# Kernel optimization log

Hardware: AMD Instinct MI355X
Metric: run time of the kernel (lower is better)

The kernel has to match this reference:

```python
import jax, jax.numpy as jnp
import numpy as np

B, H, D = 1, 24, 128
TXT, REDUX, IMG, REF, ROUTER, NC = 512, 64, 2048, 512, 32, 2
S = TXT + REDUX + IMG + REF + ROUTER
REF_SHIFT = 1.5  # model_config['ref_shift'] (nonzero to exercise the mask path)


def setup_inputs() -> dict:
    rng = jax.random.key(0)
    k1, k2, k3, k4, k5 = jax.random.split(rng, 5)
    tri = TXT + REDUX + IMG
    return {
        "query": jax.random.normal(k1, (B, H, S, D), jnp.float32),
        "key": jax.random.normal(k2, (B, H, S, D), jnp.float32),
        "value": jax.random.normal(k3, (B, H, S, D), jnp.float32),
        "ref_mask": jax.random.uniform(k4, (B, REF, tri), jnp.float32),
        "routing_map": jax.random.uniform(k5, (B, NC, IMG), jnp.float32),
        "txt_seq_len": TXT,
        "redux_seq_len": REDUX,
        "img_seq_len": IMG,
        "ref_seq_len": REF,
        "router_seq_len": ROUTER,
        "num_conds": NC,
    }


def _sdpa(q, k, v, mask=None):
    # torch F.scaled_dot_product_attention semantics (additive mask)
    scale = 1.0 / jnp.sqrt(jnp.asarray(q.shape[-1], q.dtype))
    logits = jnp.einsum('...qd,...kd->...qk', q, k) * scale
    if mask is not None:
        logits = logits + mask  # mask broadcasts over heads
    return jnp.einsum('...qk,...kd->...qd', jax.nn.softmax(logits, axis=-1), v)


def reference(query, key, value, ref_mask, routing_map,
              txt_seq_len, redux_seq_len, img_seq_len, ref_seq_len,
              router_seq_len, num_conds):
    b = query.shape[0]
    te = txt_seq_len                 # text end
    tre = te + redux_seq_len         # text+redux end
    tri = tre + img_seq_len          # text+redux+image end
    trir = tri + ref_seq_len         # +ref end

    # ---- additive attention mask (only the used [:tri, :trir] slice; broadcast over heads)
    mask = jnp.zeros((b, 1, tri, trir), query.dtype)
    mask = mask.at[:, :, :tri, tri:trir].add(REF_SHIFT)
    # ref_mask: [B, ref, tri] -> transpose -> [B, 1, tri, ref], (m-1)*100
    rm = (jnp.swapaxes(ref_mask, -1, -2)[:, None] - 1.0) * 100.0
    mask = mask.at[:, :, :tri, tri:trir].add(rm)
    # routing map for redux keys: [B, nc, img] -> repeat per-cond -> [B, redux, img] -> [B,1,img,redux]
    rep = redux_seq_len // num_conds
    redux_rt = (jnp.repeat(routing_map, rep, axis=1) - 1.0) * 100.0
    mask = mask.at[:, :, tre:tri, te:tre].add(jnp.swapaxes(redux_rt, 1, 2)[:, None])
    # routing map for ref keys: [B, nc, img] -> [B, ref, img] -> [B,1,img,ref]
    rep = ref_seq_len // num_conds
    ref_rt = (jnp.repeat(routing_map, rep, axis=1) - 1.0) * 100.0
    mask = mask.at[:, :, tre:tri, tri:trir].add(jnp.swapaxes(ref_rt, 1, 2)[:, None])

    # ---- segment 1: text+redux+image queries attend to text+redux+image+ref keys
    out1 = _sdpa(query[:, :, :tri], key[:, :, :trir], value[:, :, :trir], mask)

    # ---- segment 2: per-condition ref self-attention (block-diagonal over num_conds)
    h = query.shape[1]
    rq = query[:, :, tri:trir].reshape(b, h, num_conds, -1, D)
    rk = key[:, :, tri:trir].reshape(b, h, num_conds, -1, D)
    rv = value[:, :, tri:trir].reshape(b, h, num_conds, -1, D)
    ref_out = _sdpa(rq, rk, rv).reshape(b, h, ref_seq_len, D)

    # ---- segment 3: router queries attend to [image keys ; router keys]
    qr = query[:, :, trir:]
    kr = jnp.concatenate([key[:, :, tre:tri], key[:, :, trir:]], axis=2)
    vr = jnp.concatenate([value[:, :, tre:tri], value[:, :, trir:]], axis=2)
    router_out = _sdpa(qr, kr, vr)

    return jnp.concatenate([out1, ref_out, router_out], axis=2)
```

## Files before the change

### kernel.cpp

```cpp
#include <hip/hip_runtime.h>
#include <hip/hip_bf16.h>

#define TXT   512
#define REDUX 64
#define IMG   2048
#define REFN  512
#define NC    2
#define SEQ   3168
#define DH    128
#define NH    24
#define TRE   576
#define TRI   2624
#define TRIR  3136
#define SCALE 0.08838834764831845f
#define L2E   1.4426950408889634f
#define QSC   (SCALE * L2E)
#define C100  (100.0f * L2E)
#define CREF  (98.5f * L2E)
#define THR2  (4.0f * L2E)

using f32x4  = __attribute__((ext_vector_type(4))) float;
using short8 = __attribute__((ext_vector_type(8))) short;

__device__ inline short f2bf(float x) {
    union { __hip_bfloat16 b; short s; } u;
    u.b = __float2bfloat16(x);
    return u.s;
}

__device__ inline void gload16(const short* g, short* l) {
    __builtin_amdgcn_global_load_lds(
        (const __attribute__((address_space(1))) unsigned int*)g,
        (__attribute__((address_space(3))) unsigned int*)l, 16, 0, 0);
}

__global__ void cvt_kv_kernel(const float* __restrict__ K, const float* __restrict__ V,
                              short* __restrict__ Kb, short* __restrict__ Vt) {
    const int h   = blockIdx.y;
    const int tid = threadIdx.x;
    {
        const int base = ((h * SEQ + blockIdx.x * 16) * DH) >> 2;
        #pragma unroll
        for (int j = 0; j < 2; ++j) {
            const int i = base + tid + j * 256;
            const float4 v = ((const float4*)K)[i];
            short4 o;
            o.x = f2bf(v.x); o.y = f2bf(v.y); o.z = f2bf(v.z); o.w = f2bf(v.w);
            ((short4*)Kb)[i] = o;
        }
    }
    {
        const int s8 = blockIdx.x * 2 + (tid >> 7);
        const int d  = tid & 127;
        const int s0 = s8 * 8;
        const float* src = V + ((size_t)h * SEQ + s0) * DH + d;
        short8 w;
        #pragma unroll
        for (int j = 0; j < 8; ++j) w[j] = f2bf(src[j * DH]);
        const int tb   = s0 & ~63;
        const int j0   = s0 & 63;
        const int ks2  = j0 >> 5;
        const int jm   = j0 & 15;
        const int hi   = (j0 >> 4) & 1;
        const int pos0 = ks2 * 32 + (jm >> 2) * 8 + hi * 4;
        short* dst = Vt + ((size_t)h * DH + d) * SEQ + tb;
        short4 lo4, hi4;
        lo4.x = w[0]; lo4.y = w[1]; lo4.z = w[2]; lo4.w = w[3];
        hi4.x = w[4]; hi4.y = w[5]; hi4.z = w[6]; hi4.w = w[7];
        *(short4*)(dst + pos0)     = lo4;
        *(short4*)(dst + pos0 + 8) = hi4;
    }
}

__global__ __launch_bounds__(512, 4)
void attn_mfma(const float* __restrict__ Q, const short* __restrict__ Kb,
               const short* __restrict__ Vtg, const float* __restrict__ ref_mask,
               const float* __restrict__ routing, float* __restrict__ out)
{
    __shared__ short Ks[64 * 128];
    __shared__ short Vs[128 * 64];

    const int bid  = blockIdx.x;
    const int h    = bid % NH;
    const int bx   = bid / NH;
    const int tid  = threadIdx.x;
    const int wave = tid >> 6, lane = tid & 63;
    const int g    = lane >> 4, l4 = lane & 15;

    int qbase, ks0 = 0, ntiles;
    bool masked = false, router = false;
    if (bx < 21)       { qbase = bx * 128; ntiles = 49; masked = true; }
    else if (bx == 21) { qbase = TRIR; ntiles = 33; router = true; }
    else {
        const int b2 = bx - 22;
        qbase = TRI + b2 * 128;
        ks0 = TRI + (b2 >> 1) * 256; ntiles = 4;
    }

    const int rbase = qbase + wave * 16;
    const bool valid = !(masked && rbase >= TRI) && !(router && wave >= 2);

    const short* KbH = Kb  + (size_t)h * SEQ * DH;
    const short* VtH = Vtg + (size_t)h * DH * SEQ;
    int koff[2], vD[2], vKC[2], voff[2];
    #pragma unroll
    for (int j = 0; j < 2; ++j) {
        const int ci = tid + j * 512;
        const int kk = ci >> 4, kc = ci & 15;
        koff[j] = kk * 128 + ((kc ^ (kk & 7)) << 3);
        const int vd = ci >> 3, vk = ci & 7;
        vD[j] = vd; vKC[j] = vk;
        voff[j] = vd * SEQ + ((vk ^ (vd & 7)) << 3);
    }
    short* ksd0 = Ks + (size_t)(wave * 64) * 8;
    short* ksd1 = Ks + (size_t)(512 + wave * 64) * 8;
    short* vsd0 = Vs + (size_t)(wave * 64) * 8;
    short* vsd1 = Vs + (size_t)(512 + wave * 64) * 8;

    short8 qA[4];
    if (valid) {
        const int q = rbase + l4;
        const float* qp = Q + ((size_t)h * SEQ + q) * DH;
        #pragma unroll
        for (int ks = 0; ks < 4; ++ks) {
            const float4 a = *(const float4*)(qp + ks * 32 + g * 8);
            const float4 b = *(const float4*)(qp + ks * 32 + g * 8 + 4);
            short8 f;
            f[0] = f2bf(a.x * QSC); f[1] = f2bf(a.y * QSC);
            f[2] = f2bf(a.z * QSC); f[3] = f2bf(a.w * QSC);
            f[4] = f2bf(b.x * QSC); f[5] = f2bf(b.y * QSC);
            f[6] = f2bf(b.z * QSC); f[7] = f2bf(b.w * QSC);
            qA[ks] = f;
        }
    }

    f32x4 acc[8] = {};
    float m_run = -3.0e38f, l_run = 0.f;
    const int bsrc = (lane >> 4) << 2;

    for (int t = 0; t < ntiles; ++t) {
        const int kt = masked ? t * 64
                     : (router ? (t < 32 ? TRE + t * 64 : TRIR) : ks0 + t * 64);
        const bool tail = router && (t == 32);
        __syncthreads();
        const short* kb = KbH + (size_t)kt * DH;
        const short* vb = VtH + kt;
        {
            const int ko0 = tail ? (koff[0] & 4095) : koff[0];
            const int ko1 = tail ? (koff[1] & 4095) : koff[1];
            gload16(kb + ko0, ksd0);
            gload16(kb + ko1, ksd1);
            const int vo0 = tail ? (vD[0] * SEQ + (((vKC[0] ^ (vD[0] & 7)) & 3) << 3)) : voff[0];
            const int vo1 = tail ? (vD[1] * SEQ + (((vKC[1] ^ (vD[1] & 7)) & 3) << 3)) : voff[1];
            gload16(vb + vo0, vsd0);
            gload16(vb + vo1, vsd1);
        }
        __syncthreads();

        if (!valid) continue;

        f32x4 s[4] = {};
        __builtin_amdgcn_s_setprio(1);
        #pragma unroll
        for (int nt = 0; nt < 4; ++nt) {
            const int key = nt * 16 + l4;
            #pragma unroll
            for (int ks = 0; ks < 4; ++ks) {
                const short8 kB = *(const short8*)(Ks + key * 128 + (((ks * 4 + g) ^ (key & 7)) << 3));
                s[nt] = __builtin_amdgcn_mfma_f32_16x16x32_bf16(kB, qA[ks], s[nt], 0, 0, 0);
            }
        }
        __builtin_amdgcn_s_setprio(0);

        if (masked) {
            if (kt >= TRI) {
                const int cr = (kt - TRI) >> 8;
                const int q  = rbase + l4;
                const bool hr = rbase >= TRE;
                float radd = 0.f;
                if (hr) radd = routing[cr * IMG + (q - TRE)] * C100 - C100;
                const int j0 = kt - TRI + g * 4;
                #pragma unroll
                for (int nt = 0; nt < 4; ++nt)
                    #pragma unroll
                    for (int r = 0; r < 4; ++r) {
                        const float rmv = ref_mask[(size_t)(j0 + nt * 16 + r) * TRI + q];
                        s[nt][r] += rmv * C100 - CREF + radd;
                    }
            } else if (kt == TXT) {
                if (rbase >= TRE) {
                    const int q = rbase + l4;
                    const float a0 = routing[q - TRE] * C100 - C100;
                    const float a1 = routing[IMG + q - TRE] * C100 - C100;
                    #pragma unroll
                    for (int nt = 0; nt < 4; ++nt)
                        #pragma unroll
                        for (int r = 0; r < 4; ++r)
                            s[nt][r] += (nt >> 1) ? a1 : a0;
                }
            }
        }
        if (tail) {
            #pragma unroll
            for (int r = 0; r < 4; ++r) { s[2][r] = -3.0e38f; s[3][r] = -3.0e38f; }
        }

        float mx = fmaxf(fmaxf(s[0][0], s[0][1]), fmaxf(s[0][2], s[0][3]));
        mx = fmaxf(mx, fmaxf(fmaxf(s[1][0], s[1][1]), fmaxf(s[1][2], s[1][3])));
        mx = fmaxf(mx, fmaxf(fmaxf(s[2][0], s[2][1]), fmaxf(s[2][2], s[2][3])));
        mx = fmaxf(mx, fmaxf(fmaxf(s[3][0], s[3][1]), fmaxf(s[3][2], s[3][3])));
        mx = fmaxf(mx, __shfl_xor(mx, 16));
        mx = fmaxf(mx, __shfl_xor(mx, 32));

        if (__any(mx - m_run > THR2)) {
            const float mn    = fmaxf(m_run, mx);
            const float corrq = exp2f(m_run - mn);
            m_run = mn;
            l_run *= corrq;
            f32x4 corr;
            #pragma unroll
            for (int r = 0; r < 4; ++r) corr[r] = __shfl(corrq, bsrc + r);
            #pragma unroll
            for (int nt = 0; nt < 8; ++nt)
                #pragma unroll
                for (int r = 0; r < 4; ++r) acc[nt][r] *= corr[r];
        }

        float rsum = 0.f;
        #pragma unroll
        for (int nt = 0; nt < 4; ++nt)
            #pragma unroll
            for (int r = 0; r < 4; ++r) {
                s[nt][r] = exp2f(s[nt][r] - m_run);
                rsum += s[nt][r];
            }
        rsum += __shfl_xor(rsum, 16);
        rsum += __shfl_xor(rsum, 32);
        l_run += rsum;

        short8 pA0, pA1;
        #pragma unroll
        for (int j = 0; j < 4; ++j) {
            pA0[j]     = f2bf(s[0][j]);
            pA0[4 + j] = f2bf(s[1][j]);
            pA1[j]     = f2bf(s[2][j]);
            pA1[4 + j] = f2bf(s[3][j]);
        }

        __builtin_amdgcn_s_setprio(1);
        #pragma unroll
        for (int ks2 = 0; ks2 < 2; ++ks2) {
            const short8 pa = ks2 ? pA1 : pA0;
            const int kc = ks2 * 4 + g;
            #pragma unroll
            for (int nt = 0; nt < 8; ++nt) {
                const int d = nt * 16 + l4;
                const short8 vB = *(const short8*)(Vs + d * 64 + ((kc ^ (d & 7)) << 3));
                acc[nt] = __builtin_amdgcn_mfma_f32_16x16x32_bf16(pa, vB, acc[nt], 0, 0, 0);
            }
        }
        __builtin_amdgcn_s_setprio(0);
    }

    if (valid) {
        f32x4 linv;
        #pragma unroll
        for (int r = 0; r < 4; ++r) linv[r] = 1.0f / __shfl(l_run, bsrc + r);
        #pragma unroll
        for (int nt = 0; nt < 8; ++nt)
            #pragma unroll
            for (int r = 0; r < 4; ++r) {
                const int q = rbase + g * 4 + r;
                out[((size_t)h * SEQ + q) * DH + nt * 16 + l4] = acc[nt][r] * linv[r];
            }
    }
}

#define KT  32
#define LDK (DH + 4)
__global__ __launch_bounds__(256, 2)
void anystory_attn_scalar(const float* __restrict__ Q, const float* __restrict__ K,
                          const float* __restrict__ V, const float* __restrict__ ref_mask,
                          const float* __restrict__ routing, float* __restrict__ out, int row0)
{
    __shared__ float KsS[KT][LDK];
    __shared__ float VsS[KT][LDK];

    const int h    = blockIdx.y;
    const int r0   = row0 + blockIdx.x * 4;
    const int tid  = threadIdx.x;
    const int wave = tid >> 6;
    const int lane = tid & 63;
    const int key_l = lane & 31;
    const int half  = lane >> 5;
    const int row  = r0 + wave;

    int rs0, re0, rs1 = 0, re1 = 0;
    bool masked = false;
    if (r0 < TRI) { rs0 = 0; re0 = TRIR; masked = true; }
    else if (r0 < TRIR) {
        int c = (r0 - TRI) / (REFN / NC);
        rs0 = TRI + c * (REFN / NC); re0 = rs0 + (REFN / NC);
    } else { rs0 = TRE; re0 = TRI; rs1 = TRIR; re1 = SEQ; }

    float4 qreg[16];
    const float4* qptr = (const float4*)(Q + ((size_t)h * SEQ + row) * DH + half * 64);
    #pragma unroll
    for (int i = 0; i < 16; ++i) qreg[i] = qptr[i];

    float m = -1e30f, l = 0.f, acc0 = 0.f, acc1 = 0.f;

    for (int range = 0; range < 2; ++range) {
        const int ks = (range == 0) ? rs0 : rs1;
        const int ke = (range == 0) ? re0 : re1;
        for (int kt = ks; kt < ke; kt += KT) {
            __syncthreads();
            #pragma unroll
            for (int i = 0; i < 4; ++i) {
                int idx = tid + i * 256;
                int rr = idx >> 5, cc = (idx & 31) * 4;
                const float4 kv = ((const float4*)(K + ((size_t)h * SEQ + kt + rr) * DH))[idx & 31];
                const float4 vv = ((const float4*)(V + ((size_t)h * SEQ + kt + rr) * DH))[idx & 31];
                *(float4*)&KsS[rr][cc] = kv;
                *(float4*)&VsS[rr][cc] = vv;
            }
            __syncthreads();

            const int kglob = kt + key_l;
            float dot = 0.f;
            #pragma unroll
            for (int i = 0; i < 16; ++i) {
                float4 k4 = *(const float4*)&KsS[key_l][half * 64 + i * 4];
                dot += qreg[i].x * k4.x + qreg[i].y * k4.y + qreg[i].z * k4.z + qreg[i].w * k4.w;
            }
            dot += __shfl_xor(dot, 32);
            float logit = dot * SCALE;

            if (masked) {
                if (kglob >= TRI) {
                    logit += 1.5f + (ref_mask[(size_t)(kglob - TRI) * TRI + row] - 1.f) * 100.f;
                    if (row >= TRE)
                        logit += (routing[((kglob - TRI) >> 8) * IMG + (row - TRE)] - 1.f) * 100.f;
                } else if (kglob >= TXT && kglob < TRE && row >= TRE) {
                    logit += (routing[((kglob - TXT) >> 5) * IMG + (row - TRE)] - 1.f) * 100.f;
                }
            }

            float tm = logit;
            tm = fmaxf(tm, __shfl_xor(tm, 1));
            tm = fmaxf(tm, __shfl_xor(tm, 2));
            tm = fmaxf(tm, __shfl_xor(tm, 4));
            tm = fmaxf(tm, __shfl_xor(tm, 8));
            tm = fmaxf(tm, __shfl_xor(tm, 16));
            const float nm   = fmaxf(m, tm);
            const float corr = __expf(m - nm);
            const float p    = __expf(logit - nm);
            float ps = p;
            ps += __shfl_xor(ps, 1);
            ps += __shfl_xor(ps, 2);
            ps += __shfl_xor(ps, 4);
            ps += __shfl_xor(ps, 8);
            ps += __shfl_xor(ps, 16);
            l = l * corr + ps;
            acc0 *= corr; acc1 *= corr;
            m = nm;

            #pragma unroll
            for (int k = 0; k < KT; ++k) {
                const float pk = __shfl(p, k);
                acc0 += pk * VsS[k][lane];
                acc1 += pk * VsS[k][lane + 64];
            }
        }
    }

    const float inv = 1.f / l;
    float* op = out + ((size_t)h * SEQ + row) * DH;
    op[lane]      = acc0 * inv;
    op[lane + 64] = acc1 * inv;
}

extern "C" void kernel_launch(void* const* d_in, const int* in_sizes, int n_in,
                              void* d_out, int out_size, void* d_ws, size_t ws_size,
                              hipStream_t stream) {
    const float* Q        = (const float*)d_in[0];
    const float* K        = (const float*)d_in[1];
    const float* V        = (const float*)d_in[2];
    const float* ref_mask = (const float*)d_in[3];
    const float* routing  = (const float*)d_in[4];
    float* out = (float*)d_out;

    const size_t elems = (size_t)NH * SEQ * DH;
    const size_t need  = 2 * elems * sizeof(short);

    if (ws_size < need) {
        dim3 grid(SEQ / 4, NH);
        anystory_attn_scalar<<<grid, 256, 0, stream>>>(Q, K, V, ref_mask, routing, out, 0);
        return;
    }

    short* Kb  = (short*)d_ws;
    short* Vtg = Kb + elems;

    cvt_kv_kernel<<<dim3(SEQ / 16, NH), 256, 0, stream>>>(K, V, Kb, Vtg);

    attn_mfma<<<dim3(NH * 26), 512, 0, stream>>>(Q, Kb, Vtg, ref_mask, routing, out);
}
```

Baseline: 218.1 us.

## Split masked-segment attention over two key halves and merge partials

Splits each masked query block's 49 key tiles into two halves processed by separate workgroups. Each half writes unnormalized accumulators plus running max and sum to workspace, and a merge kernel combines them with log-sum-exp weighting. The intent is to raise the grid from 624 to 1128 blocks and shorten the longest per-block loop so the GPU's compute units are better filled. The cost is extra global traffic for roughly 64 MB of fp32 partials, one more kernel launch, and a larger workspace requirement; if the workspace is too small it falls back to the unsplit kernel.

```diff
diff --git a/kernel.cpp b/kernel.cpp
--- a/kernel.cpp
+++ b/kernel.cpp
@@ -72,10 +72,12 @@
     }
 }
 
+template<bool SPLIT>
 __global__ __launch_bounds__(512, 4)
 void attn_mfma(const float* __restrict__ Q, const short* __restrict__ Kb,
                const short* __restrict__ Vtg, const float* __restrict__ ref_mask,
-               const float* __restrict__ routing, float* __restrict__ out)
+               const float* __restrict__ routing, float* __restrict__ out,
+               float* __restrict__ accP, float* __restrict__ mP, float* __restrict__ lP)
 {
     __shared__ short Ks[64 * 128];
     __shared__ short Vs[128 * 64];
@@ -87,14 +89,21 @@
     const int wave = tid >> 6, lane = tid & 63;
     const int g    = lane >> 4, l4 = lane & 15;
 
-    int qbase, ks0 = 0, ntiles;
+    const int HB = SPLIT ? 42 : 21;
+    int qbase, ks0 = 0, t0 = 0, t1;
+    int split = 0;
     bool masked = false, router = false;
-    if (bx < 21)       { qbase = bx * 128; ntiles = 49; masked = true; }
-    else if (bx == 21) { qbase = TRIR; ntiles = 33; router = true; }
+    if (bx < HB) {
+        const int qb = SPLIT ? (bx >> 1) : bx;
+        split = SPLIT ? (bx & 1) : 0;
+        qbase = qb * 128; masked = true;
+        t0 = SPLIT ? split * 25 : 0;
+        t1 = SPLIT ? (split ? 49 : 25) : 49;
+    } else if (bx == HB) { qbase = TRIR; t1 = 33; router = true; }
     else {
-        const int b2 = bx - 22;
+        const int b2 = bx - HB - 1;
         qbase = TRI + b2 * 128;
-        ks0 = TRI + (b2 >> 1) * 256; ntiles = 4;
+        ks0 = TRI + (b2 >> 1) * 256; t1 = 4;
     }
 
     const int rbase = qbase + wave * 16;
@@ -138,7 +147,7 @@
     float m_run = -3.0e38f, l_run = 0.f;
     const int bsrc = (lane >> 4) << 2;
 
-    for (int t = 0; t < ntiles; ++t) {
+    for (int t = t0; t < t1; ++t) {
         const int kt = masked ? t * 64
                      : (router ? (t < 32 ? TRE + t * 64 : TRIR) : ks0 + t * 64);
         const bool tail = router && (t == 32);
@@ -263,17 +272,52 @@
     }
 
     if (valid) {
-        f32x4 linv;
-        #pragma unroll
-        for (int r = 0; r < 4; ++r) linv[r] = 1.0f / __shfl(l_run, bsrc + r);
-        #pragma unroll
-        for (int nt = 0; nt < 8; ++nt)
-            #pragma unroll
-            for (int r = 0; r < 4; ++r) {
-                const int q = rbase + g * 4 + r;
-                out[((size_t)h * SEQ + q) * DH + nt * 16 + l4] = acc[nt][r] * linv[r];
-            }
-    }
+        if (SPLIT && masked) {
+            float* ab = accP + ((size_t)(split * NH + h) * TRI + rbase) * DH;
+            #pragma unroll
+            for (int nt = 0; nt < 8; ++nt)
+                #pragma unroll
+                for (int r = 0; r < 4; ++r)
+                    ab[(g * 4 + r) * DH + nt * 16 + l4] = acc[nt][r];
+            if (g == 0) {
+                const size_t mi = (size_t)(split * NH + h) * TRI + rbase + l4;
+                mP[mi] = m_run;
+                lP[mi] = l_run;
+            }
+        } else {
+            f32x4 linv;
+            #pragma unroll
+            for (int r = 0; r < 4; ++r) linv[r] = 1.0f / __shfl(l_run, bsrc + r);
+            #pragma unroll
+            for (int nt = 0; nt < 8; ++nt)
+                #pragma unroll
+                for (int r = 0; r < 4; ++r) {
+                    const int q = rbase + g * 4 + r;
+                    out[((size_t)h * SEQ + q) * DH + nt * 16 + l4] = acc[nt][r] * linv[r];
+                }
+        }
+    }
+}
+
+__global__ void merge_kernel(const float* __restrict__ accP, const float* __restrict__ mP,
+                             const float* __restrict__ lP, float* __restrict__ out)
+{
+    const int idx = blockIdx.x * 256 + threadIdx.x;
+    const int c4 = idx & 31;
+    const int rowflat = idx >> 5;
+    const int h = rowflat / TRI;
+    const int q = rowflat - h * TRI;
+    const float m0 = mP[rowflat], m1 = mP[NH * TRI + rowflat];
+    const float l0 = lP[rowflat], l1 = lP[NH * TRI + rowflat];
+    const float m  = fmaxf(m0, m1);
+    const float w0 = exp2f(m0 - m), w1 = exp2f(m1 - m);
+    const float inv = 1.0f / (l0 * w0 + l1 * w1);
+    const f32x4 a0 = ((const f32x4*)accP)[(size_t)rowflat * 32 + c4];
+    const f32x4 a1 = ((const f32x4*)accP)[(size_t)(NH * TRI + rowflat) * 32 + c4];
+    f32x4 o;
+    #pragma unroll
+    for (int r = 0; r < 4; ++r) o[r] = (a0[r] * w0 + a1[r] * w1) * inv;
+    ((f32x4*)(out + ((size_t)h * SEQ + q) * DH))[c4] = o;
 }
 
 #define KT  32
@@ -390,10 +434,13 @@
     const float* routing  = (const float*)d_in[4];
     float* out = (float*)d_out;
 
-    const size_t elems = (size_t)NH * SEQ * DH;
-    const size_t need  = 2 * elems * sizeof(short);
-
-    if (ws_size < need) {
+    const size_t elems      = (size_t)NH * SEQ * DH;
+    const size_t need_base  = 2 * elems * sizeof(short);
+    const size_t acc_elems  = (size_t)2 * NH * TRI * DH;
+    const size_t ml_elems   = (size_t)2 * NH * TRI;
+    const size_t need_split = need_base + acc_elems * 4 + 2 * ml_elems * 4;
+
+    if (ws_size < need_base) {
         dim3 grid(SEQ / 4, NH);
         anystory_attn_scalar<<<grid, 256, 0, stream>>>(Q, K, V, ref_mask, routing, out, 0);
         return;
@@ -404,5 +451,15 @@
 
     cvt_kv_kernel<<<dim3(SEQ / 16, NH), 256, 0, stream>>>(K, V, Kb, Vtg);
 
-    attn_mfma<<<dim3(NH * 26), 512, 0, stream>>>(Q, Kb, Vtg, ref_mask, routing, out);
-}
+    if (ws_size >= need_split) {
+        float* accP = (float*)(Vtg + elems);
+        float* mP   = accP + acc_elems;
+        float* lP   = mP + ml_elems;
+        attn_mfma<true><<<dim3(NH * 47), 512, 0, stream>>>(Q, Kb, Vtg, ref_mask, routing,
+                                                           out, accP, mP, lP);
+        merge_kernel<<<dim3(NH * TRI * 32 / 256), 256, 0, stream>>>(accP, mP, lP, out);
+    } else {
+        attn_mfma<false><<<dim3(NH * 26), 512, 0, stream>>>(Q, Kb, Vtg, ref_mask, routing,
+                                                            out, nullptr, nullptr, nullptr);
+    }
+}
```

New measurement: 246.8 us. 1.13x slower.

## Process two 16-row query tiles per wave with 256-thread blocks

Applied to the files above, without the earlier changes.

Each wave now handles 32 query rows as two 16-row sub-tiles that share every K and V fragment read from LDS. The block shrinks from 8 to 4 waves and each thread issues four async loads per tile instead of two. The aim is to halve LDS fragment reads per MFMA and raise MFMA density per wave. In exchange, accumulator and score registers double, which may reduce occupancy, and fewer waves share each barrier-synchronised tile load.

```diff
diff --git a/kernel.cpp b/kernel.cpp
--- a/kernel.cpp
+++ b/kernel.cpp
@@ -72,7 +72,7 @@
     }
 }
 
-__global__ __launch_bounds__(512, 4)
+__global__ __launch_bounds__(256, 3)
 void attn_mfma(const float* __restrict__ Q, const short* __restrict__ Kb,
                const short* __restrict__ Vtg, const float* __restrict__ ref_mask,
                const float* __restrict__ routing, float* __restrict__ out)
@@ -97,45 +97,47 @@
         ks0 = TRI + (b2 >> 1) * 256; ntiles = 4;
     }
 
-    const int rbase = qbase + wave * 16;
-    const bool valid = !(masked && rbase >= TRI) && !(router && wave >= 2);
+    const int rbase = qbase + wave * 32;
+    const bool valid = !(masked && rbase >= TRI) && !(router && wave >= 1);
 
     const short* KbH = Kb  + (size_t)h * SEQ * DH;
     const short* VtH = Vtg + (size_t)h * DH * SEQ;
-    int koff[2], vD[2], vKC[2], voff[2];
+    int koff[4], vD[4], vKC[4], voff[4];
+    short *ksd[4], *vsd[4];
     #pragma unroll
-    for (int j = 0; j < 2; ++j) {
-        const int ci = tid + j * 512;
+    for (int j = 0; j < 4; ++j) {
+        const int ci = tid + j * 256;
         const int kk = ci >> 4, kc = ci & 15;
         koff[j] = kk * 128 + ((kc ^ (kk & 7)) << 3);
         const int vd = ci >> 3, vk = ci & 7;
         vD[j] = vd; vKC[j] = vk;
         voff[j] = vd * SEQ + ((vk ^ (vd & 7)) << 3);
-    }
-    short* ksd0 = Ks + (size_t)(wave * 64) * 8;
-    short* ksd1 = Ks + (size_t)(512 + wave * 64) * 8;
-    short* vsd0 = Vs + (size_t)(wave * 64) * 8;
-    short* vsd1 = Vs + (size_t)(512 + wave * 64) * 8;
-
-    short8 qA[4];
+        ksd[j] = Ks + (size_t)(j * 256 + wave * 64) * 8;
+        vsd[j] = Vs + (size_t)(j * 256 + wave * 64) * 8;
+    }
+
+    short8 qA[2][4];
     if (valid) {
-        const int q = rbase + l4;
-        const float* qp = Q + ((size_t)h * SEQ + q) * DH;
-        #pragma unroll
-        for (int ks = 0; ks < 4; ++ks) {
-            const float4 a = *(const float4*)(qp + ks * 32 + g * 8);
-            const float4 b = *(const float4*)(qp + ks * 32 + g * 8 + 4);
-            short8 f;
-            f[0] = f2bf(a.x * QSC); f[1] = f2bf(a.y * QSC);
-            f[2] = f2bf(a.z * QSC); f[3] = f2bf(a.w * QSC);
-            f[4] = f2bf(b.x * QSC); f[5] = f2bf(b.y * QSC);
-            f[6] = f2bf(b.z * QSC); f[7] = f2bf(b.w * QSC);
-            qA[ks] = f;
-        }
-    }
-
-    f32x4 acc[8] = {};
-    float m_run = -3.0e38f, l_run = 0.f;
+        #pragma unroll
+        for (int qt = 0; qt < 2; ++qt) {
+            const int q = rbase + qt * 16 + l4;
+            const float* qp = Q + ((size_t)h * SEQ + q) * DH;
+            #pragma unroll
+            for (int ks = 0; ks < 4; ++ks) {
+                const float4 a = *(const float4*)(qp + ks * 32 + g * 8);
+                const float4 b = *(const float4*)(qp + ks * 32 + g * 8 + 4);
+                short8 f;
+                f[0] = f2bf(a.x * QSC); f[1] = f2bf(a.y * QSC);
+                f[2] = f2bf(a.z * QSC); f[3] = f2bf(a.w * QSC);
+                f[4] = f2bf(b.x * QSC); f[5] = f2bf(b.y * QSC);
+                f[6] = f2bf(b.z * QSC); f[7] = f2bf(b.w * QSC);
+                qA[qt][ks] = f;
+            }
+        }
+    }
+
+    f32x4 acc[2][8] = {};
+    float m_run[2] = {-3.0e38f, -3.0e38f}, l_run[2] = {0.f, 0.f};
     const int bsrc = (lane >> 4) << 2;
 
     for (int t = 0; t < ntiles; ++t) {
@@ -145,21 +147,22 @@
         __syncthreads();
         const short* kb = KbH + (size_t)kt * DH;
         const short* vb = VtH + kt;
-        {
-            const int ko0 = tail ? (koff[0] & 4095) : koff[0];
-            const int ko1 = tail ? (koff[1] & 4095) : koff[1];
-            gload16(kb + ko0, ksd0);
-            gload16(kb + ko1, ksd1);
-            const int vo0 = tail ? (vD[0] * SEQ + (((vKC[0] ^ (vD[0] & 7)) & 3) << 3)) : voff[0];
-            const int vo1 = tail ? (vD[1] * SEQ + (((vKC[1] ^ (vD[1] & 7)) & 3) << 3)) : voff[1];
-            gload16(vb + vo0, vsd0);
-            gload16(vb + vo1, vsd1);
+        #pragma unroll
+        for (int j = 0; j < 4; ++j) {
+            const int ko = tail ? (koff[j] & 4095) : koff[j];
+            gload16(kb + ko, ksd[j]);
+        }
+        #pragma unroll
+        for (int j = 0; j < 4; ++j) {
+            const int vo = tail ? (vD[j] * SEQ + (((vKC[j] ^ (vD[j] & 7)) & 3) << 3))
+                                : voff[j];
+            gload16(vb + vo, vsd[j]);
         }
         __syncthreads();
 
         if (!valid) continue;
 
-        f32x4 s[4] = {};
+        f32x4 s[2][4] = {};
         __builtin_amdgcn_s_setprio(1);
         #pragma unroll
         for (int nt = 0; nt < 4; ++nt) {
@@ -167,7 +170,8 @@
             #pragma unroll
             for (int ks = 0; ks < 4; ++ks) {
                 const short8 kB = *(const short8*)(Ks + key * 128 + (((ks * 4 + g) ^ (key & 7)) << 3));
-                s[nt] = __builtin_amdgcn_mfma_f32_16x16x32_bf16(kB, qA[ks], s[nt], 0, 0, 0);
+                s[0][nt] = __builtin_amdgcn_mfma_f32_16x16x32_bf16(kB, qA[0][ks], s[0][nt], 0, 0, 0);
+                s[1][nt] = __builtin_amdgcn_mfma_f32_16x16x32_bf16(kB, qA[1][ks], s[1][nt], 0, 0, 0);
             }
         }
         __builtin_amdgcn_s_setprio(0);
@@ -175,104 +179,126 @@
         if (masked) {
             if (kt >= TRI) {
                 const int cr = (kt - TRI) >> 8;
-                const int q  = rbase + l4;
-                const bool hr = rbase >= TRE;
-                float radd = 0.f;
-                if (hr) radd = routing[cr * IMG + (q - TRE)] * C100 - C100;
                 const int j0 = kt - TRI + g * 4;
                 #pragma unroll
-                for (int nt = 0; nt < 4; ++nt)
-                    #pragma unroll
-                    for (int r = 0; r < 4; ++r) {
-                        const float rmv = ref_mask[(size_t)(j0 + nt * 16 + r) * TRI + q];
-                        s[nt][r] += rmv * C100 - CREF + radd;
-                    }
-            } else if (kt == TXT) {
-                if (rbase >= TRE) {
-                    const int q = rbase + l4;
-                    const float a0 = routing[q - TRE] * C100 - C100;
-                    const float a1 = routing[IMG + q - TRE] * C100 - C100;
+                for (int qt = 0; qt < 2; ++qt) {
+                    const int q  = rbase + qt * 16 + l4;
+                    const bool hr = rbase >= TRE;
+                    float radd = 0.f;
+                    if (hr) radd = routing[cr * IMG + (q - TRE)] * C100 - C100;
                     #pragma unroll
                     for (int nt = 0; nt < 4; ++nt)
                         #pragma unroll
-                        for (int r = 0; r < 4; ++r)
-                            s[nt][r] += (nt >> 1) ? a1 : a0;
+                        for (int r = 0; r < 4; ++r) {
+                            const float rmv = ref_mask[(size_t)(j0 + nt * 16 + r) * TRI + q];
+                            s[qt][nt][r] += rmv * C100 - CREF + radd;
+                        }
                 }
+            } else if (kt == TXT) {
+                if (rbase >= TRE) {
+                    #pragma unroll
+                    for (int qt = 0; qt < 2; ++qt) {
+                        const int q = rbase + qt * 16 + l4;
+                        const float a0 = routing[q - TRE] * C100 - C100;
+                        const float a1 = routing[IMG + q - TRE] * C100 - C100;
+                        #pragma unroll
+                        for (int nt = 0; nt < 4; ++nt)
+                            #pragma unroll
+                            for (int r = 0; r < 4; ++r)
+                                s[qt][nt][r] += (nt >> 1) ? a1 : a0;
+                    }
+                }
             }
         }
         if (tail) {
             #pragma unroll
-            for (int r = 0; r < 4; ++r) { s[2][r] = -3.0e38f; s[3][r] = -3.0e38f; }
-        }
-
-        float mx = fmaxf(fmaxf(s[0][0], s[0][1]), fmaxf(s[0][2], s[0][3]));
-        mx = fmaxf(mx, fmaxf(fmaxf(s[1][0], s[1][1]), fmaxf(s[1][2], s[1][3])));
-        mx = fmaxf(mx, fmaxf(fmaxf(s[2][0], s[2][1]), fmaxf(s[2][2], s[2][3])));
-        mx = fmaxf(mx, fmaxf(fmaxf(s[3][0], s[3][1]), fmaxf(s[3][2], s[3][3])));
-        mx = fmaxf(mx, __shfl_xor(mx, 16));
-        mx = fmaxf(mx, __shfl_xor(mx, 32));
-
-        if (__any(mx - m_run > THR2)) {
-            const float mn    = fmaxf(m_run, mx);
-            const float corrq = exp2f(m_run - mn);
-            m_run = mn;
-            l_run *= corrq;
-            f32x4 corr;
-            #pragma unroll
-            for (int r = 0; r < 4; ++r) corr[r] = __shfl(corrq, bsrc + r);
-            #pragma unroll
-            for (int nt = 0; nt < 8; ++nt)
-                #pragma unroll
-                for (int r = 0; r < 4; ++r) acc[nt][r] *= corr[r];
-        }
-
-        float rsum = 0.f;
-        #pragma unroll
-        for (int nt = 0; nt < 4; ++nt)
-            #pragma unroll
-            for (int r = 0; r < 4; ++r) {
-                s[nt][r] = exp2f(s[nt][r] - m_run);
-                rsum += s[nt][r];
-            }
-        rsum += __shfl_xor(rsum, 16);
-        rsum += __shfl_xor(rsum, 32);
-        l_run += rsum;
-
-        short8 pA0, pA1;
-        #pragma unroll
-        for (int j = 0; j < 4; ++j) {
-            pA0[j]     = f2bf(s[0][j]);
-            pA0[4 + j] = f2bf(s[1][j]);
-            pA1[j]     = f2bf(s[2][j]);
-            pA1[4 + j] = f2bf(s[3][j]);
+            for (int qt = 0; qt < 2; ++qt)
+                #pragma unroll
+                for (int r = 0; r < 4; ++r) { s[qt][2][r] = -3.0e38f; s[qt][3][r] = -3.0e38f; }
+        }
+
+        float mx[2];
+        #pragma unroll
+        for (int qt = 0; qt < 2; ++qt) {
+            float m0 = fmaxf(fmaxf(s[qt][0][0], s[qt][0][1]), fmaxf(s[qt][0][2], s[qt][0][3]));
+            m0 = fmaxf(m0, fmaxf(fmaxf(s[qt][1][0], s[qt][1][1]), fmaxf(s[qt][1][2], s[qt][1][3])));
+            m0 = fmaxf(m0, fmaxf(fmaxf(s[qt][2][0], s[qt][2][1]), fmaxf(s[qt][2][2], s[qt][2][3])));
+            m0 = fmaxf(m0, fmaxf(fmaxf(s[qt][3][0], s[qt][3][1]), fmaxf(s[qt][3][2], s[qt][3][3])));
+            m0 = fmaxf(m0, __shfl_xor(m0, 16));
+            m0 = fmaxf(m0, __shfl_xor(m0, 32));
+            mx[qt] = m0;
+        }
+
+        const float gmax = fmaxf(mx[0] - m_run[0], mx[1] - m_run[1]);
+        if (__any(gmax > THR2)) {
+            #pragma unroll
+            for (int qt = 0; qt < 2; ++qt) {
+                const float mn    = fmaxf(m_run[qt], mx[qt]);
+                const float corrq = exp2f(m_run[qt] - mn);
+                m_run[qt] = mn;
+                l_run[qt] *= corrq;
+                f32x4 corr;
+                #pragma unroll
+                for (int r = 0; r < 4; ++r) corr[r] = __shfl(corrq, bsrc + r);
+                #pragma unroll
+                for (int nt = 0; nt < 8; ++nt)
+                    #pragma unroll
+                    for (int r = 0; r < 4; ++r) acc[qt][nt][r] *= corr[r];
+            }
+        }
+
+        short8 pA[2][2];
+        #pragma unroll
+        for (int qt = 0; qt < 2; ++qt) {
+            float rsum = 0.f;
+            #pragma unroll
+            for (int nt = 0; nt < 4; ++nt)
+                #pragma unroll
+                for (int r = 0; r < 4; ++r) {
+                    s[qt][nt][r] = exp2f(s[qt][nt][r] - m_run[qt]);
+                    rsum += s[qt][nt][r];
+                }
+            rsum += __shfl_xor(rsum, 16);
+            rsum += __shfl_xor(rsum, 32);
+            l_run[qt] += rsum;
+            #pragma unroll
+            for (int j = 0; j < 4; ++j) {
+                pA[qt][0][j]     = f2bf(s[qt][0][j]);
+                pA[qt][0][4 + j] = f2bf(s[qt][1][j]);
+                pA[qt][1][j]     = f2bf(s[qt][2][j]);
+                pA[qt][1][4 + j] = f2bf(s[qt][3][j]);
+            }
         }
 
         __builtin_amdgcn_s_setprio(1);
         #pragma unroll
         for (int ks2 = 0; ks2 < 2; ++ks2) {
-            const short8 pa = ks2 ? pA1 : pA0;
             const int kc = ks2 * 4 + g;
             #pragma unroll
             for (int nt = 0; nt < 8; ++nt) {
                 const int d = nt * 16 + l4;
                 const short8 vB = *(const short8*)(Vs + d * 64 + ((kc ^ (d & 7)) << 3));
-                acc[nt] = __builtin_amdgcn_mfma_f32_16x16x32_bf16(pa, vB, acc[nt], 0, 0, 0);
+                acc[0][nt] = __builtin_amdgcn_mfma_f32_16x16x32_bf16(pA[0][ks2], vB, acc[0][nt], 0, 0, 0);
+                acc[1][nt] = __builtin_amdgcn_mfma_f32_16x16x32_bf16(pA[1][ks2], vB, acc[1][nt], 0, 0, 0);
             }
         }
         __builtin_amdgcn_s_setprio(0);
     }
 
     if (valid) {
-        f32x4 linv;
-        #pragma unroll
-        for (int r = 0; r < 4; ++r) linv[r] = 1.0f / __shfl(l_run, bsrc + r);
-        #pragma unroll
-        for (int nt = 0; nt < 8; ++nt)
-            #pragma unroll
-            for (int r = 0; r < 4; ++r) {
-                const int q = rbase + g * 4 + r;
-                out[((size_t)h * SEQ + q) * DH + nt * 16 + l4] = acc[nt][r] * linv[r];
-            }
+        #pragma unroll
+        for (int qt = 0; qt < 2; ++qt) {
+            f32x4 linv;
+            #pragma unroll
+            for (int r = 0; r < 4; ++r) linv[r] = 1.0f / __shfl(l_run[qt], bsrc + r);
+            #pragma unroll
+            for (int nt = 0; nt < 8; ++nt)
+                #pragma unroll
+                for (int r = 0; r < 4; ++r) {
+                    const int q = rbase + qt * 16 + g * 4 + r;
+                    out[((size_t)h * SEQ + q) * DH + nt * 16 + l4] = acc[qt][nt][r] * linv[r];
+                }
+        }
     }
 }
 
@@ -404,5 +430,5 @@
 
     cvt_kv_kernel<<<dim3(SEQ / 16, NH), 256, 0, stream>>>(K, V, Kb, Vtg);
 
-    attn_mfma<<<dim3(NH * 26), 512, 0, stream>>>(Q, Kb, Vtg, ref_mask, routing, out);
-}
+    attn_mfma<<<dim3(NH * 26), 256, 0, stream>>>(Q, Kb, Vtg, ref_mask, routing, out);
+}
```

Measured after the change: 317.9 us. 45.8% more time.
